# Kernel optimization log

Hardware: AMD Instinct MI355X
Metric: run time of the kernel (lower is better)

Reference implementation:

```python
import jax, jax.numpy as jnp
import numpy as np

NEG_INF = -1e9  # masked_fill value from the torch module


def setup_inputs() -> dict:
    key = jax.random.key(0)
    ks = jax.random.split(key, 6)
    n_edges, hidden = 100000, 256
    n_paths, max_len = 20000, 16
    edge_emb = jax.random.normal(ks[0], (n_edges, hidden), dtype=jnp.float32)
    paths = jax.random.randint(ks[1], (n_paths, max_len), 0, n_edges)
    path_lens = jax.random.randint(ks[2], (n_paths,), 0, max_len)  # +1 in reference -> 1..max_len
    path_mask = jax.random.randint(ks[3], (n_paths,), 0, 2)
    # nn.Linear(hidden, 1) parameters
    W = jax.random.normal(ks[4], (1, hidden), dtype=jnp.float32) / np.sqrt(hidden)
    b = jax.random.normal(ks[5], (1,), dtype=jnp.float32) * 0.01
    return {"edge_emb": edge_emb, "paths": paths, "path_lens": path_lens,
            "path_mask": path_mask, "W": W, "b": b, "deterministic": 1}


def reference(edge_emb, paths, path_lens, path_mask, W, b, deterministic):
    # ragged per-path mean: emulate `for p in paths: edge_emb[p].mean(0)` with padded gather
    lens = path_lens + 1                                   # [P], 1..max_len
    pos = jnp.arange(paths.shape[1])                        # [L]
    valid = pos[None, :] < lens[:, None]                    # [P, L]
    gathered = edge_emb[paths]                              # [P, L, H]
    z = jnp.sum(jnp.where(valid[..., None], gathered, 0.0), axis=1) / lens[:, None].astype(edge_emb.dtype)  # [P, H]
    logits = z @ W[0] + b[0]                                # [P]  (Linear(H,1).squeeze())
    logits = jnp.where(path_mask == 0, NEG_INF, logits)
    logp = jax.nn.log_softmax(logits)
    if deterministic:
        p = jnp.argmax(logits)
    else:
        p = jax.random.categorical(jax.random.key(42), logits)
    logprob = logp[p]
    return (p, logprob, z[p])
```

## Files before the change

### kernel.cpp

```cpp
#include <hip/hip_runtime.h>
#include <math.h>
#include <limits.h>

#define NEG_INF -1e9f

__global__ __launch_bounds__(256) void k_edge_dot(
    const float* __restrict__ emb, const float* __restrict__ W,
    float* __restrict__ s, int* __restrict__ counter, int n_edges)
{
    if (blockIdx.x == 0 && threadIdx.x == 0) *counter = 0;
    int wave = (blockIdx.x * (int)blockDim.x + (int)threadIdx.x) >> 6;
    int lane = threadIdx.x & 63;
    if (wave >= n_edges) return;
    const float4 e = ((const float4*)emb)[(size_t)wave * 64 + lane];
    const float4 w = ((const float4*)W)[lane];
    float d = e.x * w.x + e.y * w.y + e.z * w.z + e.w * w.w;
#pragma unroll
    for (int off = 32; off; off >>= 1) d += __shfl_down(d, off, 64);
    if (lane == 0) s[wave] = d;
}

__global__ __launch_bounds__(256) void k_fused_slot(
    const float* __restrict__ s, const int* __restrict__ paths,
    const int* __restrict__ path_lens, const int* __restrict__ path_mask,
    const float* __restrict__ b, const float* __restrict__ emb,
    float* __restrict__ pmax, int* __restrict__ pidx, float* __restrict__ psum,
    int* __restrict__ counter, float* __restrict__ out,
    int n_paths, int max_len)
{
    __shared__ float bl[16];  __shared__ int bix[16];
    __shared__ float rv[4];   __shared__ int ri[4];   __shared__ float rs[4];
    __shared__ float s_M, s_S; __shared__ int s_P, s_last;

    const int tid = threadIdx.x, lane = tid & 63, wv = tid >> 6;
    const int t = blockIdx.x * 256 + tid;
    const int p = t >> 4, slot = t & 15;

    float val = 0.f; int mask = 0, len = 1;
    const int inb = (p < n_paths);
    if (inb) {
        mask = path_mask[p];
        len  = path_lens[p] + 1;
        if (mask && slot < len) val = s[paths[t]];
    }
#pragma unroll
    for (int m = 1; m <= 8; m <<= 1) val += __shfl_xor(val, m, 16);
    if (slot == 0) {
        bl[tid >> 4]  = inb ? (mask ? val / (float)len + b[0] : NEG_INF)
                            : -INFINITY;
        bix[tid >> 4] = inb ? p : INT_MAX;
    }
    __syncthreads();

    if (tid == 0) {
        float bm = -INFINITY; int bi = INT_MAX;
        for (int i = 0; i < 16; ++i)
            if (bl[i] > bm || (bl[i] == bm && bix[i] < bi)) { bm = bl[i]; bi = bix[i]; }
        float bs = 0.f;
        if (bi != INT_MAX)
            for (int i = 0; i < 16; ++i)
                if (bix[i] != INT_MAX) bs += expf(bl[i] - bm);
        pmax[blockIdx.x] = bm;
        pidx[blockIdx.x] = bi;
        psum[blockIdx.x] = bs;
        __threadfence();
        int tk = atomicAdd(counter, 1);
        s_last = (tk == (int)gridDim.x - 1) ? 1 : 0;
    }
    __syncthreads();
    if (!s_last) return;
    __threadfence();

    const int nb = gridDim.x;
    float mv = -INFINITY; int mi = INT_MAX;
    for (int i = tid; i < nb; i += 256) {
        float tv = pmax[i]; int ti = pidx[i];
        if (tv > mv || (tv == mv && ti < mi)) { mv = tv; mi = ti; }
    }
#pragma unroll
    for (int off = 32; off; off >>= 1) {
        float ov = __shfl_down(mv, off, 64);
        int   oi = __shfl_down(mi, off, 64);
        if (ov > mv || (ov == mv && oi < mi)) { mv = ov; mi = oi; }
    }
    if (lane == 0) { rv[wv] = mv; ri[wv] = mi; }
    __syncthreads();
    if (tid == 0) {
        float M = rv[0]; int P = ri[0];
        for (int w = 1; w < 4; ++w)
            if (rv[w] > M || (rv[w] == M && ri[w] < P)) { M = rv[w]; P = ri[w]; }
        s_M = M; s_P = P;
    }
    __syncthreads();
    const float M = s_M; const int P = s_P;

    float sp = 0.f;
    for (int i = tid; i < nb; i += 256)
        sp += psum[i] * expf(pmax[i] - M);
#pragma unroll
    for (int off = 32; off; off >>= 1) sp += __shfl_down(sp, off, 64);
    if (lane == 0) rs[wv] = sp;
    __syncthreads();
    if (tid == 0) s_S = rs[0] + rs[1] + rs[2] + rs[3];
    __syncthreads();

    const int lenP = path_lens[P] + 1;
    const int* pp = paths + (size_t)P * max_len;
    float acc = 0.f;
    for (int j = 0; j < lenP; ++j)
        acc += emb[(size_t)pp[j] * 256 + tid];
    out[2 + tid] = acc / (float)lenP;
    if (tid == 0) { out[0] = (float)P; out[1] = -logf(s_S); }
}


__global__ __launch_bounds__(256) void k_fused_gen(
    const float* __restrict__ s, const int* __restrict__ paths,
    const int* __restrict__ path_lens, const int* __restrict__ path_mask,
    const float* __restrict__ b, const float* __restrict__ emb,
    float* __restrict__ pmax, int* __restrict__ pidx, float* __restrict__ psum,
    int* __restrict__ counter, float* __restrict__ out,
    int n_paths, int max_len)
{
    __shared__ float rv[4]; __shared__ int ri[4]; __shared__ float rs[4];
    __shared__ float s_M, s_S; __shared__ int s_P, s_last;

    const int tid = threadIdx.x, lane = tid & 63, wv = tid >> 6;
    const int p = blockIdx.x * 256 + tid;

    float v = -INFINITY; int vi = INT_MAX;
    if (p < n_paths) {
        vi = p;
        if (path_mask[p] == 0) v = NEG_INF;
        else {
            int len = path_lens[p] + 1;
            const int* pp = paths + (size_t)p * max_len;
            float acc = 0.f;
            for (int j = 0; j < len; ++j) acc += s[pp[j]];
            v = acc / (float)len + b[0];
        }
    }
    float bv = v; int bi = vi;
#pragma unroll
    for (int off = 32; off; off >>= 1) {
        float ov = __shfl_down(bv, off, 64);
        int   oi = __shfl_down(bi, off, 64);
        if (ov > bv || (ov == bv && oi < bi)) { bv = ov; bi = oi; }
    }
    if (lane == 0) { rv[wv] = bv; ri[wv] = bi; }
    __syncthreads();
    if (tid == 0) {
        float mvv = rv[0]; int mii = ri[0];
        for (int w = 1; w < 4; ++w)
            if (rv[w] > mvv || (rv[w] == mvv && ri[w] < mii)) { mvv = rv[w]; mii = ri[w]; }
        s_M = mvv; s_P = mii;
    }
    __syncthreads();
    const float bm = s_M;
    float se = expf(v - bm);
#pragma unroll
    for (int off = 32; off; off >>= 1) se += __shfl_down(se, off, 64);
    if (lane == 0) rs[wv] = se;
    __syncthreads();
    if (tid == 0) {
        pmax[blockIdx.x] = bm;
        pidx[blockIdx.x] = s_P;
        psum[blockIdx.x] = rs[0] + rs[1] + rs[2] + rs[3];
        __threadfence();
        int tk = atomicAdd(counter, 1);
        s_last = (tk == (int)gridDim.x - 1) ? 1 : 0;
    }
    __syncthreads();
    if (!s_last) return;
    __threadfence();

    const int nb = gridDim.x;
    float mv = -INFINITY; int mi = INT_MAX;
    for (int i = tid; i < nb; i += 256) {
        float tv = pmax[i]; int ti = pidx[i];
        if (tv > mv || (tv == mv && ti < mi)) { mv = tv; mi = ti; }
    }
#pragma unroll
    for (int off = 32; off; off >>= 1) {
        float ov = __shfl_down(mv, off, 64);
        int   oi = __shfl_down(mi, off, 64);
        if (ov > mv || (ov == mv && oi < mi)) { mv = ov; mi = oi; }
    }
    if (lane == 0) { rv[wv] = mv; ri[wv] = mi; }
    __syncthreads();
    if (tid == 0) {
        float M = rv[0]; int P = ri[0];
        for (int w = 1; w < 4; ++w)
            if (rv[w] > M || (rv[w] == M && ri[w] < P)) { M = rv[w]; P = ri[w]; }
        s_M = M; s_P = P;
    }
    __syncthreads();
    const float M = s_M; const int P = s_P;
    float sp = 0.f;
    for (int i = tid; i < nb; i += 256)
        sp += psum[i] * expf(pmax[i] - M);
#pragma unroll
    for (int off = 32; off; off >>= 1) sp += __shfl_down(sp, off, 64);
    if (lane == 0) rs[wv] = sp;
    __syncthreads();
    if (tid == 0) s_S = rs[0] + rs[1] + rs[2] + rs[3];
    __syncthreads();

    const int lenP = path_lens[P] + 1;
    const int* pp = paths + (size_t)P * max_len;
    if (tid < 256) {
        float acc = 0.f;
        for (int j = 0; j < lenP; ++j)
            acc += emb[(size_t)pp[j] * 256 + tid];
        out[2 + tid] = acc / (float)lenP;
    }
    if (tid == 0) { out[0] = (float)P; out[1] = -logf(s_S); }
}


extern "C" void kernel_launch(void* const* d_in, const int* in_sizes, int n_in,
                              void* d_out, int out_size, void* d_ws, size_t ws_size,
                              hipStream_t stream) {
    const float* emb       = (const float*)d_in[0];
    const int*   paths     = (const int*)  d_in[1];
    const int*   path_lens = (const int*)  d_in[2];
    const int*   path_mask = (const int*)  d_in[3];
    const float* W         = (const float*)d_in[4];
    const float* b         = (const float*)d_in[5];

    int hidden  = in_sizes[4];
    int n_edges = in_sizes[0] / hidden;
    int n_paths = in_sizes[2];
    int max_len = in_sizes[1] / n_paths;

    float* s = (float*)d_ws;

    if (max_len == 16 && hidden == 256) {
        int nb2 = (n_paths * 16 + 255) / 256;
        float* pmax    = s + n_edges;
        float* psum    = pmax + nb2;
        int*   pidx    = (int*)(psum + nb2);
        int*   counter = pidx + nb2;

        int blocks1 = (n_edges * 64 + 255) / 256;
        k_edge_dot<<<blocks1, 256, 0, stream>>>(emb, W, s, counter, n_edges);
        k_fused_slot<<<nb2, 256, 0, stream>>>(s, paths, path_lens, path_mask,
                                              b, emb, pmax, pidx, psum, counter,
                                              (float*)d_out, n_paths, max_len);
    } else {
        int blocks2 = (n_paths + 255) / 256;
        float* pmax    = s + n_edges;
        float* psum    = pmax + blocks2;
        int*   pidx    = (int*)(psum + blocks2);
        int*   counter = pidx + blocks2;

        int blocks1 = (n_edges * 64 + 255) / 256;
        k_edge_dot<<<blocks1, 256, 0, stream>>>(emb, W, s, counter, n_edges);
        k_fused_gen<<<blocks2, 256, 0, stream>>>(s, paths, path_lens, path_mask,
                                                 b, emb, pmax, pidx, psum, counter,
                                                 (float*)d_out, n_paths, max_len);
    }
}
```

Before: 190.4 us.

## Merge edge-dot and path reduction into one cooperative persistent kernel

Replaces the two-kernel sequence (per-edge dot product, then per-path slot reduction with an atomic last-block finalize) with a single cooperative kernel of 256 persistent blocks. Grid-wide syncs separate three phases: edge dots with four edges per wave, per-thread path gathers through int4 index loads, and a final block-0 reduction plus gathering of the winning path's embedding. This removes one kernel launch and the atomic counter, and gives more loads in flight per wave. The cost is only 256 blocks to stream the 100 MB embedding table, plus grid.sync overhead.

```diff
diff --git a/kernel.cpp b/kernel.cpp
--- a/kernel.cpp
+++ b/kernel.cpp
@@ -1,8 +1,150 @@
 #include <hip/hip_runtime.h>
+#include <hip/hip_cooperative_groups.h>
 #include <math.h>
 #include <limits.h>
 
+namespace cg = cooperative_groups;
+
 #define NEG_INF -1e9f
+
+__global__ __launch_bounds__(256) void k_coop(
+    const float* __restrict__ emb, const int* __restrict__ paths,
+    const int* __restrict__ path_lens, const int* __restrict__ path_mask,
+    const float* __restrict__ W, const float* __restrict__ b,
+    float* __restrict__ s, float* __restrict__ pmax, int* __restrict__ pidx,
+    float* __restrict__ psum, float* __restrict__ out,
+    int n_edges, int n_paths, int max_len)
+{
+    cg::grid_group grid = cg::this_grid();
+
+    __shared__ float rv[4]; __shared__ int ri[4]; __shared__ float rs[4];
+    __shared__ float s_M, s_S; __shared__ int s_P;
+
+    const int tid  = threadIdx.x, lane = tid & 63, wv = tid >> 6;
+    const int nblk = (int)gridDim.x;
+    const int gwave = blockIdx.x * 4 + wv;
+    const int nwave = nblk * 4;
+
+    {
+        const float4  w4   = ((const float4*)W)[lane];
+        const float4* emb4 = (const float4*)emb;
+        for (int base = gwave * 4; base < n_edges; base += nwave * 4) {
+            const int v1 = base + 1 < n_edges, v2 = base + 2 < n_edges,
+                      v3 = base + 3 < n_edges;
+            float4 r0 = emb4[(size_t)base * 64 + lane];
+            float4 r1 = v1 ? emb4[(size_t)(base + 1) * 64 + lane] : make_float4(0,0,0,0);
+            float4 r2 = v2 ? emb4[(size_t)(base + 2) * 64 + lane] : make_float4(0,0,0,0);
+            float4 r3 = v3 ? emb4[(size_t)(base + 3) * 64 + lane] : make_float4(0,0,0,0);
+            float d0 = r0.x*w4.x + r0.y*w4.y + r0.z*w4.z + r0.w*w4.w;
+            float d1 = r1.x*w4.x + r1.y*w4.y + r1.z*w4.z + r1.w*w4.w;
+            float d2 = r2.x*w4.x + r2.y*w4.y + r2.z*w4.z + r2.w*w4.w;
+            float d3 = r3.x*w4.x + r3.y*w4.y + r3.z*w4.z + r3.w*w4.w;
+#pragma unroll
+            for (int off = 32; off; off >>= 1) {
+                d0 += __shfl_down(d0, off, 64);
+                d1 += __shfl_down(d1, off, 64);
+                d2 += __shfl_down(d2, off, 64);
+                d3 += __shfl_down(d3, off, 64);
+            }
+            if (lane == 0) {
+                s[base] = d0;
+                if (v1) s[base + 1] = d1;
+                if (v2) s[base + 2] = d2;
+                if (v3) s[base + 3] = d3;
+            }
+        }
+    }
+    grid.sync();
+
+    {
+        const int p = blockIdx.x + nblk * tid;
+        float v = -INFINITY; int vi = INT_MAX;
+        if (p < n_paths) {
+            vi = p;
+            if (path_mask[p] == 0) v = NEG_INF;
+            else {
+                const int len = path_lens[p] + 1;
+                const int4* pp4 = (const int4*)(paths + (size_t)p * 16);
+                int4 a0 = pp4[0], a1 = pp4[1], a2 = pp4[2], a3 = pp4[3];
+                int idx[16] = { a0.x, a0.y, a0.z, a0.w, a1.x, a1.y, a1.z, a1.w,
+                                a2.x, a2.y, a2.z, a2.w, a3.x, a3.y, a3.z, a3.w };
+                float acc = 0.f;
+#pragma unroll
+                for (int j = 0; j < 16; ++j) {
+                    float t = s[idx[j]];
+                    acc += (j < len) ? t : 0.f;
+                }
+                v = acc / (float)len + b[0];
+            }
+        }
+        float bv = v; int bi = vi;
+#pragma unroll
+        for (int off = 32; off; off >>= 1) {
+            float ov = __shfl_down(bv, off, 64);
+            int   oi = __shfl_down(bi, off, 64);
+            if (ov > bv || (ov == bv && oi < bi)) { bv = ov; bi = oi; }
+        }
+        if (lane == 0) { rv[wv] = bv; ri[wv] = bi; }
+        __syncthreads();
+        if (tid == 0) {
+            float bm = rv[0]; int bmi = ri[0];
+            for (int w = 1; w < 4; ++w)
+                if (rv[w] > bm || (rv[w] == bm && ri[w] < bmi)) { bm = rv[w]; bmi = ri[w]; }
+            s_M = bm; s_P = bmi;
+        }
+        __syncthreads();
+        const float bm = s_M;
+        float se = (vi == INT_MAX) ? 0.f : expf(v - bm);
+#pragma unroll
+        for (int off = 32; off; off >>= 1) se += __shfl_down(se, off, 64);
+        if (lane == 0) rs[wv] = se;
+        __syncthreads();
+        if (tid == 0) {
+            pmax[blockIdx.x] = s_M;
+            pidx[blockIdx.x] = s_P;
+            psum[blockIdx.x] = rs[0] + rs[1] + rs[2] + rs[3];
+        }
+    }
+    grid.sync();
+    if (blockIdx.x != 0) return;
+
+    {
+        float mv = pmax[tid]; int mi = pidx[tid];
+#pragma unroll
+        for (int off = 32; off; off >>= 1) {
+            float ov = __shfl_down(mv, off, 64);
+            int   oi = __shfl_down(mi, off, 64);
+            if (ov > mv || (ov == mv && oi < mi)) { mv = ov; mi = oi; }
+        }
+        if (lane == 0) { rv[wv] = mv; ri[wv] = mi; }
+        __syncthreads();
+        if (tid == 0) {
+            float M = rv[0]; int P = ri[0];
+            for (int w = 1; w < 4; ++w)
+                if (rv[w] > M || (rv[w] == M && ri[w] < P)) { M = rv[w]; P = ri[w]; }
+            s_M = M; s_P = P;
+        }
+        __syncthreads();
+        const float M = s_M; const int P = s_P;
+
+        float sp = psum[tid] * expf(pmax[tid] - M);
+#pragma unroll
+        for (int off = 32; off; off >>= 1) sp += __shfl_down(sp, off, 64);
+        if (lane == 0) rs[wv] = sp;
+        __syncthreads();
+        if (tid == 0) s_S = rs[0] + rs[1] + rs[2] + rs[3];
+        __syncthreads();
+
+        const int lenP = path_lens[P] + 1;
+        const int* pp = paths + (size_t)P * max_len;
+        float acc = 0.f;
+        for (int j = 0; j < lenP; ++j)
+            acc += emb[(size_t)pp[j] * 256 + tid];
+        out[2 + tid] = acc / (float)lenP;
+        if (tid == 0) { out[0] = (float)P; out[1] = -logf(s_S); }
+    }
+}
+
 
 __global__ __launch_bounds__(256) void k_edge_dot(
     const float* __restrict__ emb, const float* __restrict__ W,
@@ -20,100 +162,6 @@
     if (lane == 0) s[wave] = d;
 }
 
-__global__ __launch_bounds__(256) void k_fused_slot(
-    const float* __restrict__ s, const int* __restrict__ paths,
-    const int* __restrict__ path_lens, const int* __restrict__ path_mask,
-    const float* __restrict__ b, const float* __restrict__ emb,
-    float* __restrict__ pmax, int* __restrict__ pidx, float* __restrict__ psum,
-    int* __restrict__ counter, float* __restrict__ out,
-    int n_paths, int max_len)
-{
-    __shared__ float bl[16];  __shared__ int bix[16];
-    __shared__ float rv[4];   __shared__ int ri[4];   __shared__ float rs[4];
-    __shared__ float s_M, s_S; __shared__ int s_P, s_last;
-
-    const int tid = threadIdx.x, lane = tid & 63, wv = tid >> 6;
-    const int t = blockIdx.x * 256 + tid;
-    const int p = t >> 4, slot = t & 15;
-
-    float val = 0.f; int mask = 0, len = 1;
-    const int inb = (p < n_paths);
-    if (inb) {
-        mask = path_mask[p];
-        len  = path_lens[p] + 1;
-        if (mask && slot < len) val = s[paths[t]];
-    }
-#pragma unroll
-    for (int m = 1; m <= 8; m <<= 1) val += __shfl_xor(val, m, 16);
-    if (slot == 0) {
-        bl[tid >> 4]  = inb ? (mask ? val / (float)len + b[0] : NEG_INF)
-                            : -INFINITY;
-        bix[tid >> 4] = inb ? p : INT_MAX;
-    }
-    __syncthreads();
-
-    if (tid == 0) {
-        float bm = -INFINITY; int bi = INT_MAX;
-        for (int i = 0; i < 16; ++i)
-            if (bl[i] > bm || (bl[i] == bm && bix[i] < bi)) { bm = bl[i]; bi = bix[i]; }
-        float bs = 0.f;
-        if (bi != INT_MAX)
-            for (int i = 0; i < 16; ++i)
-                if (bix[i] != INT_MAX) bs += expf(bl[i] - bm);
-        pmax[blockIdx.x] = bm;
-        pidx[blockIdx.x] = bi;
-        psum[blockIdx.x] = bs;
-        __threadfence();
-        int tk = atomicAdd(counter, 1);
-        s_last = (tk == (int)gridDim.x - 1) ? 1 : 0;
-    }
-    __syncthreads();
-    if (!s_last) return;
-    __threadfence();
-
-    const int nb = gridDim.x;
-    float mv = -INFINITY; int mi = INT_MAX;
-    for (int i = tid; i < nb; i += 256) {
-        float tv = pmax[i]; int ti = pidx[i];
-        if (tv > mv || (tv == mv && ti < mi)) { mv = tv; mi = ti; }
-    }
-#pragma unroll
-    for (int off = 32; off; off >>= 1) {
-        float ov = __shfl_down(mv, off, 64);
-        int   oi = __shfl_down(mi, off, 64);
-        if (ov > mv || (ov == mv && oi < mi)) { mv = ov; mi = oi; }
-    }
-    if (lane == 0) { rv[wv] = mv; ri[wv] = mi; }
-    __syncthreads();
-    if (tid == 0) {
-        float M = rv[0]; int P = ri[0];
-        for (int w = 1; w < 4; ++w)
-            if (rv[w] > M || (rv[w] == M && ri[w] < P)) { M = rv[w]; P = ri[w]; }
-        s_M = M; s_P = P;
-    }
-    __syncthreads();
-    const float M = s_M; const int P = s_P;
-
-    float sp = 0.f;
-    for (int i = tid; i < nb; i += 256)
-        sp += psum[i] * expf(pmax[i] - M);
-#pragma unroll
-    for (int off = 32; off; off >>= 1) sp += __shfl_down(sp, off, 64);
-    if (lane == 0) rs[wv] = sp;
-    __syncthreads();
-    if (tid == 0) s_S = rs[0] + rs[1] + rs[2] + rs[3];
-    __syncthreads();
-
-    const int lenP = path_lens[P] + 1;
-    const int* pp = paths + (size_t)P * max_len;
-    float acc = 0.f;
-    for (int j = 0; j < lenP; ++j)
-        acc += emb[(size_t)pp[j] * 256 + tid];
-    out[2 + tid] = acc / (float)lenP;
-    if (tid == 0) { out[0] = (float)P; out[1] = -logf(s_S); }
-}
-
-
 __global__ __launch_bounds__(256) void k_fused_gen(
     const float* __restrict__ s, const int* __restrict__ paths,
     const int* __restrict__ path_lens, const int* __restrict__ path_mask,
@@ -236,17 +284,19 @@
     float* s = (float*)d_ws;
 
     if (max_len == 16 && hidden == 256) {
-        int nb2 = (n_paths * 16 + 255) / 256;
-        float* pmax    = s + n_edges;
-        float* psum    = pmax + nb2;
-        int*   pidx    = (int*)(psum + nb2);
-        int*   counter = pidx + nb2;
-
-        int blocks1 = (n_edges * 64 + 255) / 256;
-        k_edge_dot<<<blocks1, 256, 0, stream>>>(emb, W, s, counter, n_edges);
-        k_fused_slot<<<nb2, 256, 0, stream>>>(s, paths, path_lens, path_mask,
-                                              b, emb, pmax, pidx, psum, counter,
-                                              (float*)d_out, n_paths, max_len);
+        const int nblk = 256;
+        float* pmax = s + n_edges;
+        float* psum = pmax + nblk;
+        int*   pidx = (int*)(psum + nblk);
+        float* outp = (float*)d_out;
+
+        void* args[] = { (void*)&emb, (void*)&paths, (void*)&path_lens,
+                         (void*)&path_mask, (void*)&W, (void*)&b,
+                         (void*)&s, (void*)&pmax, (void*)&pidx, (void*)&psum,
+                         (void*)&outp, (void*)&n_edges, (void*)&n_paths,
+                         (void*)&max_len };
+        hipLaunchCooperativeKernel((const void*)k_coop, dim3(nblk), dim3(256),
+                                   args, 0, stream);
     } else {
         int blocks2 = (n_paths + 255) / 256;
         float* pmax    = s + n_edges;
```

Measured after the change: 243.4 us. 27.8% more time.
